# Optimization experiments

Hardware: AMD Instinct MI355X
Metric: run time of the kernel (lower is better)

Reference implementation:

```python
import jax, jax.numpy as jnp
import numpy as np

B, N = 256, 16384


def setup_inputs() -> dict:
    key = jax.random.key(0)
    k1, k2, k3 = jax.random.split(key, 3)
    pred_coords = jax.random.normal(k1, (B, N, 3), dtype=jnp.float32)
    true_coords = jax.random.normal(k2, (B, N, 3), dtype=jnp.float32)
    weights = jax.random.uniform(k3, (B, N), dtype=jnp.float32)
    mask = jnp.ones((B, N), dtype=bool)
    return {"pred_coords": pred_coords, "true_coords": true_coords,
            "weights": weights, "mask": mask}


def reference(pred_coords, true_coords, weights, mask):
    # Mask out invalid atoms (Algorithm 28, weighted Kabsch alignment)
    pred = jnp.where(mask[..., None], pred_coords, 0.0)
    true = jnp.where(mask[..., None], true_coords, 0.0)
    w = jnp.where(mask, weights, 0.0)[..., None]            # [b, n, 1]

    wsum = w.sum(axis=1, keepdims=True)                     # [b, 1, 1]
    pred_centroid = (pred * w).sum(axis=1, keepdims=True) / wsum
    true_centroid = (true * w).sum(axis=1, keepdims=True) / wsum

    pred_c = pred - pred_centroid                           # [b, n, 3]
    true_c = true - true_centroid                           # [b, n, 3]

    # weighted covariance: [b, 3, 3]
    cov = jnp.einsum('bni,bnj->bij', true_c * w, pred_c)

    # torch.svd returns V (not V^T); jnp returns Vh = V^T. rot = U @ V^T = U @ Vh
    U, _, Vh = jnp.linalg.svd(cov)
    rot = jnp.einsum('bij,bjk->bik', U, Vh)

    # reflection fix: flip last column of V (= last row of Vh) where det < 0
    det = jnp.linalg.det(rot)                               # [b]
    flip = jnp.where(det < 0, -1.0, 1.0)                    # [b]
    Vh_fixed = Vh.at[:, -1, :].multiply(flip[:, None])
    rot = jnp.einsum('bij,bjk->bik', U, Vh_fixed)

    aligned = jnp.einsum('bni,bij->bnj', pred_c, rot) + true_centroid
    # original module calls .detach_() on the output
    return jax.lax.stop_gradient(aligned)
```

## Files before the change

### kernel.cpp

```cpp
#include <hip/hip_runtime.h>
#include <stdint.h>
#include <math.h>

constexpr int BATCH  = 256;
constexpr int NATOM  = 16384;
constexpr int CHUNKS = 16;
constexpr int TPB    = 256;
constexpr int APT    = 4;
constexpr int NQ     = 16;

__global__ __launch_bounds__(TPB) void wra_partials(
    const float* __restrict__ pred, const float* __restrict__ tru,
    const float* __restrict__ wgt, const int* __restrict__ mask,
    float* __restrict__ partials)
{
    const int blk = blockIdx.x;
    const int b   = blk >> 4;
    const int s   = blk & 15;
    const int tid = threadIdx.x;
    const long base = (long)b * NATOM + (long)s * (TPB * APT) + (long)tid * APT;

    const float4* p4 = reinterpret_cast<const float4*>(pred + base * 3);
    const float4* t4 = reinterpret_cast<const float4*>(tru  + base * 3);
    float4 pA = p4[0], pB = p4[1], pC = p4[2];
    float4 tA = t4[0], tB = t4[1], tC = t4[2];
    float4 wv = *reinterpret_cast<const float4*>(wgt + base);
    int4   mv = *reinterpret_cast<const int4*>(mask + base);

    float P[12] = {pA.x,pA.y,pA.z,pA.w, pB.x,pB.y,pB.z,pB.w, pC.x,pC.y,pC.z,pC.w};
    float T[12] = {tA.x,tA.y,tA.z,tA.w, tB.x,tB.y,tB.z,tB.w, tC.x,tC.y,tC.z,tC.w};
    float W[4]  = {mv.x ? wv.x : 0.f, mv.y ? wv.y : 0.f,
                   mv.z ? wv.z : 0.f, mv.w ? wv.w : 0.f};

    float acc[NQ];
    #pragma unroll
    for (int k = 0; k < NQ; ++k) acc[k] = 0.f;

    #pragma unroll
    for (int k = 0; k < APT; ++k) {
        float w  = W[k];
        float px = P[3*k], py = P[3*k+1], pz = P[3*k+2];
        float tx = T[3*k], ty = T[3*k+1], tz = T[3*k+2];
        float wtx = w * tx, wty = w * ty, wtz = w * tz;
        acc[0]  += w;
        acc[1]  += w * px;  acc[2]  += w * py;  acc[3]  += w * pz;
        acc[4]  += wtx;     acc[5]  += wty;     acc[6]  += wtz;
        acc[7]  += wtx*px;  acc[8]  += wtx*py;  acc[9]  += wtx*pz;
        acc[10] += wty*px;  acc[11] += wty*py;  acc[12] += wty*pz;
        acc[13] += wtz*px;  acc[14] += wtz*py;  acc[15] += wtz*pz;
    }

    #pragma unroll
    for (int off = 32; off > 0; off >>= 1) {
        #pragma unroll
        for (int k = 0; k < NQ; ++k)
            acc[k] += __shfl_down(acc[k], off, 64);
    }
    __shared__ float red[4][NQ];
    const int wave = tid >> 6, lane = tid & 63;
    if (lane == 0) {
        #pragma unroll
        for (int k = 0; k < NQ; ++k) red[wave][k] = acc[k];
    }
    __syncthreads();
    if (tid < NQ)
        partials[blk * NQ + tid] =
            red[0][tid] + red[1][tid] + red[2][tid] + red[3][tid];
}

__device__ inline void jrot(double M[3][3], double V[3][3], int p, int q) {
    double mpq = M[p][q];
    if (fabs(mpq) < 1e-300) return;
    double theta = (M[q][q] - M[p][p]) / (2.0 * mpq);
    double t = copysign(1.0, theta) / (fabs(theta) + sqrt(theta * theta + 1.0));
    double c = 1.0 / sqrt(t * t + 1.0);
    double s = t * c;
    int r = 3 - p - q;
    double mpp = M[p][p], mqq = M[q][q], mrp = M[r][p], mrq = M[r][q];
    M[p][p] = mpp - t * mpq;
    M[q][q] = mqq + t * mpq;
    M[p][q] = M[q][p] = 0.0;
    double nrp = c * mrp - s * mrq;
    double nrq = s * mrp + c * mrq;
    M[r][p] = M[p][r] = nrp;
    M[r][q] = M[q][r] = nrq;
    #pragma unroll
    for (int i = 0; i < 3; ++i) {
        double vip = V[i][p], viq = V[i][q];
        V[i][p] = c * vip - s * viq;
        V[i][q] = s * vip + c * viq;
    }
}

__global__ __launch_bounds__(64) void wra_solve(
    const float* __restrict__ partials, float* __restrict__ consts)
{
    const int b = blockIdx.x, tid = threadIdx.x;
    __shared__ double q[NQ];
    if (tid < NQ) {
        double sum = 0.0;
        for (int s = 0; s < CHUNKS; ++s)
            sum += (double)partials[(b * CHUNKS + s) * NQ + tid];
        q[tid] = sum;
    }
    __syncthreads();
    if (tid != 0) return;

    double wsum = q[0];
    double pc[3], tc[3];
    for (int j = 0; j < 3; ++j) { pc[j] = q[1+j] / wsum; tc[j] = q[4+j] / wsum; }

    double C[3][3];
    for (int i = 0; i < 3; ++i)
        for (int j = 0; j < 3; ++j)
            C[i][j] = q[7 + 3*i + j] - wsum * tc[i] * pc[j];

    double M[3][3];
    for (int i = 0; i < 3; ++i)
        for (int j = 0; j < 3; ++j)
            M[i][j] = C[0][i]*C[0][j] + C[1][i]*C[1][j] + C[2][i]*C[2][j];
    double V[3][3] = {{1,0,0},{0,1,0},{0,0,1}};
    for (int sweep = 0; sweep < 12; ++sweep) {
        double off = M[0][1]*M[0][1] + M[0][2]*M[0][2] + M[1][2]*M[1][2];
        double diag = M[0][0] + M[1][1] + M[2][2];
        if (off <= 1e-28 * diag * diag) break;
        jrot(M, V, 0, 1);
        jrot(M, V, 0, 2);
        jrot(M, V, 1, 2);
    }
    double lam[3] = {M[0][0], M[1][1], M[2][2]};
    int i0 = 0, i1 = 1, i2 = 2, tmp;
    if (lam[i0] < lam[i1]) { tmp = i0; i0 = i1; i1 = tmp; }
    if (lam[i0] < lam[i2]) { tmp = i0; i0 = i2; i2 = tmp; }
    if (lam[i1] < lam[i2]) { tmp = i1; i1 = i2; i2 = tmp; }
    double v0[3] = {V[0][i0], V[1][i0], V[2][i0]};
    double v1[3] = {V[0][i1], V[1][i1], V[2][i1]};
    double v2[3] = {V[0][i2], V[1][i2], V[2][i2]};

    double u0[3], u1[3];
    for (int i = 0; i < 3; ++i) {
        u0[i] = C[i][0]*v0[0] + C[i][1]*v0[1] + C[i][2]*v0[2];
        u1[i] = C[i][0]*v1[0] + C[i][1]*v1[1] + C[i][2]*v1[2];
    }
    double n0 = sqrt(u0[0]*u0[0] + u0[1]*u0[1] + u0[2]*u0[2]);
    for (int i = 0; i < 3; ++i) u0[i] /= n0;
    double d01 = u1[0]*u0[0] + u1[1]*u0[1] + u1[2]*u0[2];
    for (int i = 0; i < 3; ++i) u1[i] -= d01 * u0[i];
    double n1 = sqrt(u1[0]*u1[0] + u1[1]*u1[1] + u1[2]*u1[2]);
    for (int i = 0; i < 3; ++i) u1[i] /= n1;

    double detV = v0[0]*(v1[1]*v2[2] - v1[2]*v2[1])
                - v0[1]*(v1[0]*v2[2] - v1[2]*v2[0])
                + v0[2]*(v1[0]*v2[1] - v1[1]*v2[0]);
    double sV = (detV >= 0.0) ? 1.0 : -1.0;
    double u2[3] = { sV * (u0[1]*u1[2] - u0[2]*u1[1]),
                     sV * (u0[2]*u1[0] - u0[0]*u1[2]),
                     sV * (u0[0]*u1[1] - u0[1]*u1[0]) };

    float* out = consts + b * 15;
    for (int i = 0; i < 3; ++i)
        for (int j = 0; j < 3; ++j)
            out[3*i + j] = (float)(u0[i]*v0[j] + u1[i]*v1[j] + u2[i]*v2[j]);
    for (int j = 0; j < 3; ++j) { out[9 + j] = (float)pc[j]; out[12 + j] = (float)tc[j]; }
}

__global__ __launch_bounds__(TPB) void wra_apply(
    const float* __restrict__ pred, const int* __restrict__ mask,
    const float* __restrict__ consts, float* __restrict__ out)
{
    const int blk = blockIdx.x;
    const int b   = blk >> 4;
    const int s   = blk & 15;
    const int tid = threadIdx.x;

    __shared__ float c[15];
    if (tid < 15) c[tid] = consts[b * 15 + tid];
    __syncthreads();

    const long base = (long)b * NATOM + (long)s * (TPB * APT) + (long)tid * APT;
    const float4* p4 = reinterpret_cast<const float4*>(pred + base * 3);
    float4 pA = p4[0], pB = p4[1], pC = p4[2];
    int4   mv = *reinterpret_cast<const int4*>(mask + base);

    float P[12] = {pA.x,pA.y,pA.z,pA.w, pB.x,pB.y,pB.z,pB.w, pC.x,pC.y,pC.z,pC.w};
    int Mk[4] = {mv.x, mv.y, mv.z, mv.w};
    float O[12];

    #pragma unroll
    for (int k = 0; k < APT; ++k) {
        float px = (Mk[k] ? P[3*k]   : 0.f) - c[9];
        float py = (Mk[k] ? P[3*k+1] : 0.f) - c[10];
        float pz = (Mk[k] ? P[3*k+2] : 0.f) - c[11];
        O[3*k]   = px * c[0] + py * c[3] + pz * c[6] + c[12];
        O[3*k+1] = px * c[1] + py * c[4] + pz * c[7] + c[13];
        O[3*k+2] = px * c[2] + py * c[5] + pz * c[8] + c[14];
    }
    float4* o4 = reinterpret_cast<float4*>(out + base * 3);
    o4[0] = make_float4(O[0], O[1], O[2],  O[3]);
    o4[1] = make_float4(O[4], O[5], O[6],  O[7]);
    o4[2] = make_float4(O[8], O[9], O[10], O[11]);
}

extern "C" void kernel_launch(void* const* d_in, const int* in_sizes, int n_in,
                              void* d_out, int out_size, void* d_ws, size_t ws_size,
                              hipStream_t stream) {
    const float* pred = (const float*)d_in[0];
    const float* tru  = (const float*)d_in[1];
    const float* wgt  = (const float*)d_in[2];
    const int*   mask = (const int*)d_in[3];
    float* out = (float*)d_out;

    float* partials = (float*)d_ws;
    float* consts   = partials + BATCH * CHUNKS * NQ;

    hipLaunchKernelGGL(wra_partials, dim3(BATCH * CHUNKS), dim3(TPB), 0, stream,
                       pred, tru, wgt, mask, partials);
    hipLaunchKernelGGL(wra_solve, dim3(BATCH), dim3(64), 0, stream,
                       partials, consts);
    hipLaunchKernelGGL(wra_apply, dim3(BATCH * CHUNKS), dim3(TPB), 0, stream,
                       pred, mask, consts, out);
}
```

Baseline: 186.5 us.

## Fuse reduce, solve and apply into one kernel per batch, keeping pred in registers

Replaces the three-kernel pipeline with a single kernel per batch element of 1024 threads. Each thread loads 16 atoms, accumulates the moments and keeps the masked pred coordinates in registers. A thread-0 Jacobi solve runs in shared memory, and then the same threads apply the rotation without re-reading pred or mask. This removes the global partials round trip, two kernel launches and the second read of pred and mask. In exchange only 256 blocks are launched, roughly one per CU, and all other threads of a block sit idle during the serial double-precision solve, so memory-level parallelism and overlap may drop.

Result: slower. 194.7 us (+4.4%).

```diff
diff --git a/kernel.cpp b/kernel.cpp
--- a/kernel.cpp
+++ b/kernel.cpp
@@ -4,69 +4,11 @@
 
 constexpr int BATCH  = 256;
 constexpr int NATOM  = 16384;
-constexpr int CHUNKS = 16;
-constexpr int TPB    = 256;
-constexpr int APT    = 4;
+constexpr int TPB    = 1024;
+constexpr int GROUPS = 4;
 constexpr int NQ     = 16;
-
-__global__ __launch_bounds__(TPB) void wra_partials(
-    const float* __restrict__ pred, const float* __restrict__ tru,
-    const float* __restrict__ wgt, const int* __restrict__ mask,
-    float* __restrict__ partials)
-{
-    const int blk = blockIdx.x;
-    const int b   = blk >> 4;
-    const int s   = blk & 15;
-    const int tid = threadIdx.x;
-    const long base = (long)b * NATOM + (long)s * (TPB * APT) + (long)tid * APT;
-
-    const float4* p4 = reinterpret_cast<const float4*>(pred + base * 3);
-    const float4* t4 = reinterpret_cast<const float4*>(tru  + base * 3);
-    float4 pA = p4[0], pB = p4[1], pC = p4[2];
-    float4 tA = t4[0], tB = t4[1], tC = t4[2];
-    float4 wv = *reinterpret_cast<const float4*>(wgt + base);
-    int4   mv = *reinterpret_cast<const int4*>(mask + base);
-
-    float P[12] = {pA.x,pA.y,pA.z,pA.w, pB.x,pB.y,pB.z,pB.w, pC.x,pC.y,pC.z,pC.w};
-    float T[12] = {tA.x,tA.y,tA.z,tA.w, tB.x,tB.y,tB.z,tB.w, tC.x,tC.y,tC.z,tC.w};
-    float W[4]  = {mv.x ? wv.x : 0.f, mv.y ? wv.y : 0.f,
-                   mv.z ? wv.z : 0.f, mv.w ? wv.w : 0.f};
-
-    float acc[NQ];
-    #pragma unroll
-    for (int k = 0; k < NQ; ++k) acc[k] = 0.f;
-
-    #pragma unroll
-    for (int k = 0; k < APT; ++k) {
-        float w  = W[k];
-        float px = P[3*k], py = P[3*k+1], pz = P[3*k+2];
-        float tx = T[3*k], ty = T[3*k+1], tz = T[3*k+2];
-        float wtx = w * tx, wty = w * ty, wtz = w * tz;
-        acc[0]  += w;
-        acc[1]  += w * px;  acc[2]  += w * py;  acc[3]  += w * pz;
-        acc[4]  += wtx;     acc[5]  += wty;     acc[6]  += wtz;
-        acc[7]  += wtx*px;  acc[8]  += wtx*py;  acc[9]  += wtx*pz;
-        acc[10] += wty*px;  acc[11] += wty*py;  acc[12] += wty*pz;
-        acc[13] += wtz*px;  acc[14] += wtz*py;  acc[15] += wtz*pz;
-    }
-
-    #pragma unroll
-    for (int off = 32; off > 0; off >>= 1) {
-        #pragma unroll
-        for (int k = 0; k < NQ; ++k)
-            acc[k] += __shfl_down(acc[k], off, 64);
-    }
-    __shared__ float red[4][NQ];
-    const int wave = tid >> 6, lane = tid & 63;
-    if (lane == 0) {
-        #pragma unroll
-        for (int k = 0; k < NQ; ++k) red[wave][k] = acc[k];
-    }
-    __syncthreads();
-    if (tid < NQ)
-        partials[blk * NQ + tid] =
-            red[0][tid] + red[1][tid] + red[2][tid] + red[3][tid];
-}
+constexpr int NWAVE  = TPB / 64;
+
 
 __device__ inline void jrot(double M[3][3], double V[3][3], int p, int q) {
     double mpq = M[p][q];
@@ -76,10 +18,10 @@
     double c = 1.0 / sqrt(t * t + 1.0);
     double s = t * c;
     int r = 3 - p - q;
-    double mpp = M[p][p], mqq = M[q][q], mrp = M[r][p], mrq = M[r][q];
-    M[p][p] = mpp - t * mpq;
-    M[q][q] = mqq + t * mpq;
+    M[p][p] -= t * mpq;
+    M[q][q] += t * mpq;
     M[p][q] = M[q][p] = 0.0;
+    double mrp = M[r][p], mrq = M[r][q];
     double nrp = c * mrp - s * mrq;
     double nrq = s * mrp + c * mrq;
     M[r][p] = M[p][r] = nrp;
@@ -92,113 +34,162 @@
     }
 }
 
-__global__ __launch_bounds__(64) void wra_solve(
-    const float* __restrict__ partials, float* __restrict__ consts)
+__global__ __launch_bounds__(TPB) void wra_fused(
+    const float* __restrict__ pred, const float* __restrict__ tru,
+    const float* __restrict__ wgt, const int* __restrict__ mask,
+    float* __restrict__ out)
 {
-    const int b = blockIdx.x, tid = threadIdx.x;
-    __shared__ double q[NQ];
+    const int b   = blockIdx.x;
+    const int tid = threadIdx.x;
+    const long batch0 = (long)b * NATOM;
+
+    float MP[GROUPS][12];
+    float acc[NQ];
+    #pragma unroll
+    for (int k = 0; k < NQ; ++k) acc[k] = 0.f;
+
+    #pragma unroll
+    for (int g = 0; g < GROUPS; ++g) {
+        const long base = batch0 + (long)g * (TPB * 4) + (long)tid * 4;
+        const float4* p4 = reinterpret_cast<const float4*>(pred + base * 3);
+        const float4* t4 = reinterpret_cast<const float4*>(tru  + base * 3);
+        float4 pA = p4[0], pB = p4[1], pC = p4[2];
+        float4 tA = t4[0], tB = t4[1], tC = t4[2];
+        float4 wv = *reinterpret_cast<const float4*>(wgt + base);
+        int4   mv = *reinterpret_cast<const int4*>(mask + base);
+
+        float P[12] = {pA.x,pA.y,pA.z,pA.w, pB.x,pB.y,pB.z,pB.w, pC.x,pC.y,pC.z,pC.w};
+        float T[12] = {tA.x,tA.y,tA.z,tA.w, tB.x,tB.y,tB.z,tB.w, tC.x,tC.y,tC.z,tC.w};
+        int   Mk[4] = {mv.x, mv.y, mv.z, mv.w};
+        float W[4]  = {Mk[0] ? wv.x : 0.f, Mk[1] ? wv.y : 0.f,
+                       Mk[2] ? wv.z : 0.f, Mk[3] ? wv.w : 0.f};
+
+        #pragma unroll
+        for (int k = 0; k < 4; ++k) {
+            float px = Mk[k] ? P[3*k]   : 0.f;
+            float py = Mk[k] ? P[3*k+1] : 0.f;
+            float pz = Mk[k] ? P[3*k+2] : 0.f;
+            MP[g][3*k] = px; MP[g][3*k+1] = py; MP[g][3*k+2] = pz;
+            float w  = W[k];
+            float tx = T[3*k], ty = T[3*k+1], tz = T[3*k+2];
+            float wtx = w * tx, wty = w * ty, wtz = w * tz;
+            acc[0]  += w;
+            acc[1]  += w * px;  acc[2]  += w * py;  acc[3]  += w * pz;
+            acc[4]  += wtx;     acc[5]  += wty;     acc[6]  += wtz;
+            acc[7]  += wtx*px;  acc[8]  += wtx*py;  acc[9]  += wtx*pz;
+            acc[10] += wty*px;  acc[11] += wty*py;  acc[12] += wty*pz;
+            acc[13] += wtz*px;  acc[14] += wtz*py;  acc[15] += wtz*pz;
+        }
+    }
+
+    #pragma unroll
+    for (int off = 32; off > 0; off >>= 1) {
+        #pragma unroll
+        for (int k = 0; k < NQ; ++k)
+            acc[k] += __shfl_down(acc[k], off, 64);
+    }
+    __shared__ float red[NWAVE][NQ];
+    __shared__ double qd[NQ];
+    __shared__ float sc[15];
+    const int wave = tid >> 6, lane = tid & 63;
+    if (lane == 0) {
+        #pragma unroll
+        for (int k = 0; k < NQ; ++k) red[wave][k] = acc[k];
+    }
+    __syncthreads();
     if (tid < NQ) {
         double sum = 0.0;
-        for (int s = 0; s < CHUNKS; ++s)
-            sum += (double)partials[(b * CHUNKS + s) * NQ + tid];
-        q[tid] = sum;
+        #pragma unroll
+        for (int w = 0; w < NWAVE; ++w) sum += (double)red[w][tid];
+        qd[tid] = sum;
     }
     __syncthreads();
-    if (tid != 0) return;
-
-    double wsum = q[0];
-    double pc[3], tc[3];
-    for (int j = 0; j < 3; ++j) { pc[j] = q[1+j] / wsum; tc[j] = q[4+j] / wsum; }
-
-    double C[3][3];
-    for (int i = 0; i < 3; ++i)
-        for (int j = 0; j < 3; ++j)
-            C[i][j] = q[7 + 3*i + j] - wsum * tc[i] * pc[j];
-
-    double M[3][3];
-    for (int i = 0; i < 3; ++i)
-        for (int j = 0; j < 3; ++j)
-            M[i][j] = C[0][i]*C[0][j] + C[1][i]*C[1][j] + C[2][i]*C[2][j];
-    double V[3][3] = {{1,0,0},{0,1,0},{0,0,1}};
-    for (int sweep = 0; sweep < 12; ++sweep) {
-        double off = M[0][1]*M[0][1] + M[0][2]*M[0][2] + M[1][2]*M[1][2];
-        double diag = M[0][0] + M[1][1] + M[2][2];
-        if (off <= 1e-28 * diag * diag) break;
-        jrot(M, V, 0, 1);
-        jrot(M, V, 0, 2);
-        jrot(M, V, 1, 2);
-    }
-    double lam[3] = {M[0][0], M[1][1], M[2][2]};
-    int i0 = 0, i1 = 1, i2 = 2, tmp;
-    if (lam[i0] < lam[i1]) { tmp = i0; i0 = i1; i1 = tmp; }
-    if (lam[i0] < lam[i2]) { tmp = i0; i0 = i2; i2 = tmp; }
-    if (lam[i1] < lam[i2]) { tmp = i1; i1 = i2; i2 = tmp; }
-    double v0[3] = {V[0][i0], V[1][i0], V[2][i0]};
-    double v1[3] = {V[0][i1], V[1][i1], V[2][i1]};
-    double v2[3] = {V[0][i2], V[1][i2], V[2][i2]};
-
-    double u0[3], u1[3];
-    for (int i = 0; i < 3; ++i) {
-        u0[i] = C[i][0]*v0[0] + C[i][1]*v0[1] + C[i][2]*v0[2];
-        u1[i] = C[i][0]*v1[0] + C[i][1]*v1[1] + C[i][2]*v1[2];
-    }
-    double n0 = sqrt(u0[0]*u0[0] + u0[1]*u0[1] + u0[2]*u0[2]);
-    for (int i = 0; i < 3; ++i) u0[i] /= n0;
-    double d01 = u1[0]*u0[0] + u1[1]*u0[1] + u1[2]*u0[2];
-    for (int i = 0; i < 3; ++i) u1[i] -= d01 * u0[i];
-    double n1 = sqrt(u1[0]*u1[0] + u1[1]*u1[1] + u1[2]*u1[2]);
-    for (int i = 0; i < 3; ++i) u1[i] /= n1;
-
-    double detV = v0[0]*(v1[1]*v2[2] - v1[2]*v2[1])
-                - v0[1]*(v1[0]*v2[2] - v1[2]*v2[0])
-                + v0[2]*(v1[0]*v2[1] - v1[1]*v2[0]);
-    double sV = (detV >= 0.0) ? 1.0 : -1.0;
-    double u2[3] = { sV * (u0[1]*u1[2] - u0[2]*u1[1]),
-                     sV * (u0[2]*u1[0] - u0[0]*u1[2]),
-                     sV * (u0[0]*u1[1] - u0[1]*u1[0]) };
-
-    float* out = consts + b * 15;
-    for (int i = 0; i < 3; ++i)
-        for (int j = 0; j < 3; ++j)
-            out[3*i + j] = (float)(u0[i]*v0[j] + u1[i]*v1[j] + u2[i]*v2[j]);
-    for (int j = 0; j < 3; ++j) { out[9 + j] = (float)pc[j]; out[12 + j] = (float)tc[j]; }
-}
-
-__global__ __launch_bounds__(TPB) void wra_apply(
-    const float* __restrict__ pred, const int* __restrict__ mask,
-    const float* __restrict__ consts, float* __restrict__ out)
-{
-    const int blk = blockIdx.x;
-    const int b   = blk >> 4;
-    const int s   = blk & 15;
-    const int tid = threadIdx.x;
-
-    __shared__ float c[15];
-    if (tid < 15) c[tid] = consts[b * 15 + tid];
+
+    if (tid == 0) {
+        double q[NQ];
+        for (int k = 0; k < NQ; ++k) q[k] = qd[k];
+        double wsum = q[0];
+        double pc[3], tc[3];
+        for (int j = 0; j < 3; ++j) { pc[j] = q[1+j] / wsum; tc[j] = q[4+j] / wsum; }
+
+        double C[3][3];
+        for (int i = 0; i < 3; ++i)
+            for (int j = 0; j < 3; ++j)
+                C[i][j] = q[7 + 3*i + j] - wsum * tc[i] * pc[j];
+
+        double M[3][3];
+        for (int i = 0; i < 3; ++i)
+            for (int j = 0; j < 3; ++j)
+                M[i][j] = C[0][i]*C[0][j] + C[1][i]*C[1][j] + C[2][i]*C[2][j];
+        double V[3][3] = {{1,0,0},{0,1,0},{0,0,1}};
+        for (int sweep = 0; sweep < 12; ++sweep) {
+            double off = M[0][1]*M[0][1] + M[0][2]*M[0][2] + M[1][2]*M[1][2];
+            double diag = M[0][0] + M[1][1] + M[2][2];
+            if (off <= 1e-28 * diag * diag) break;
+            jrot(M, V, 0, 1);
+            jrot(M, V, 0, 2);
+            jrot(M, V, 1, 2);
+        }
+        double lam[3] = {M[0][0], M[1][1], M[2][2]};
+        int i0 = 0, i1 = 1, i2 = 2, tmp;
+        if (lam[i0] < lam[i1]) { tmp = i0; i0 = i1; i1 = tmp; }
+        if (lam[i0] < lam[i2]) { tmp = i0; i0 = i2; i2 = tmp; }
+        if (lam[i1] < lam[i2]) { tmp = i1; i1 = i2; i2 = tmp; }
+        double v0[3] = {V[0][i0], V[1][i0], V[2][i0]};
+        double v1[3] = {V[0][i1], V[1][i1], V[2][i1]};
+        double v2[3] = {V[0][i2], V[1][i2], V[2][i2]};
+
+        double u0[3], u1[3];
+        for (int i = 0; i < 3; ++i) {
+            u0[i] = C[i][0]*v0[0] + C[i][1]*v0[1] + C[i][2]*v0[2];
+            u1[i] = C[i][0]*v1[0] + C[i][1]*v1[1] + C[i][2]*v1[2];
+        }
+        double n0 = sqrt(u0[0]*u0[0] + u0[1]*u0[1] + u0[2]*u0[2]);
+        for (int i = 0; i < 3; ++i) u0[i] /= n0;
+        double d01 = u1[0]*u0[0] + u1[1]*u0[1] + u1[2]*u0[2];
+        for (int i = 0; i < 3; ++i) u1[i] -= d01 * u0[i];
+        double n1 = sqrt(u1[0]*u1[0] + u1[1]*u1[1] + u1[2]*u1[2]);
+        for (int i = 0; i < 3; ++i) u1[i] /= n1;
+
+        double detV = v0[0]*(v1[1]*v2[2] - v1[2]*v2[1])
+                    - v0[1]*(v1[0]*v2[2] - v1[2]*v2[0])
+                    + v0[2]*(v1[0]*v2[1] - v1[1]*v2[0]);
+        double sV = (detV >= 0.0) ? 1.0 : -1.0;
+        double u2[3] = { sV * (u0[1]*u1[2] - u0[2]*u1[1]),
+                         sV * (u0[2]*u1[0] - u0[0]*u1[2]),
+                         sV * (u0[0]*u1[1] - u0[1]*u1[0]) };
+
+        for (int i = 0; i < 3; ++i)
+            for (int j = 0; j < 3; ++j)
+                sc[3*i + j] = (float)(u0[i]*v0[j] + u1[i]*v1[j] + u2[i]*v2[j]);
+        for (int j = 0; j < 3; ++j) { sc[9 + j] = (float)pc[j]; sc[12 + j] = (float)tc[j]; }
+    }
     __syncthreads();
 
-    const long base = (long)b * NATOM + (long)s * (TPB * APT) + (long)tid * APT;
-    const float4* p4 = reinterpret_cast<const float4*>(pred + base * 3);
-    float4 pA = p4[0], pB = p4[1], pC = p4[2];
-    int4   mv = *reinterpret_cast<const int4*>(mask + base);
-
-    float P[12] = {pA.x,pA.y,pA.z,pA.w, pB.x,pB.y,pB.z,pB.w, pC.x,pC.y,pC.z,pC.w};
-    int Mk[4] = {mv.x, mv.y, mv.z, mv.w};
-    float O[12];
-
-    #pragma unroll
-    for (int k = 0; k < APT; ++k) {
-        float px = (Mk[k] ? P[3*k]   : 0.f) - c[9];
-        float py = (Mk[k] ? P[3*k+1] : 0.f) - c[10];
-        float pz = (Mk[k] ? P[3*k+2] : 0.f) - c[11];
-        O[3*k]   = px * c[0] + py * c[3] + pz * c[6] + c[12];
-        O[3*k+1] = px * c[1] + py * c[4] + pz * c[7] + c[13];
-        O[3*k+2] = px * c[2] + py * c[5] + pz * c[8] + c[14];
-    }
-    float4* o4 = reinterpret_cast<float4*>(out + base * 3);
-    o4[0] = make_float4(O[0], O[1], O[2],  O[3]);
-    o4[1] = make_float4(O[4], O[5], O[6],  O[7]);
-    o4[2] = make_float4(O[8], O[9], O[10], O[11]);
+    const float c0 = sc[0], c1 = sc[1], c2 = sc[2],
+                c3 = sc[3], c4 = sc[4], c5 = sc[5],
+                c6 = sc[6], c7 = sc[7], c8 = sc[8],
+                pcx = sc[9], pcy = sc[10], pcz = sc[11],
+                tcx = sc[12], tcy = sc[13], tcz = sc[14];
+
+    #pragma unroll
+    for (int g = 0; g < GROUPS; ++g) {
+        const long base = batch0 + (long)g * (TPB * 4) + (long)tid * 4;
+        float O[12];
+        #pragma unroll
+        for (int k = 0; k < 4; ++k) {
+            float px = MP[g][3*k]   - pcx;
+            float py = MP[g][3*k+1] - pcy;
+            float pz = MP[g][3*k+2] - pcz;
+            O[3*k]   = px * c0 + py * c3 + pz * c6 + tcx;
+            O[3*k+1] = px * c1 + py * c4 + pz * c7 + tcy;
+            O[3*k+2] = px * c2 + py * c5 + pz * c8 + tcz;
+        }
+        float4* o4 = reinterpret_cast<float4*>(out + base * 3);
+        o4[0] = make_float4(O[0], O[1], O[2],  O[3]);
+        o4[1] = make_float4(O[4], O[5], O[6],  O[7]);
+        o4[2] = make_float4(O[8], O[9], O[10], O[11]);
+    }
 }
 
 extern "C" void kernel_launch(void* const* d_in, const int* in_sizes, int n_in,
@@ -210,13 +201,6 @@
     const int*   mask = (const int*)d_in[3];
     float* out = (float*)d_out;
 
-    float* partials = (float*)d_ws;
-    float* consts   = partials + BATCH * CHUNKS * NQ;
-
-    hipLaunchKernelGGL(wra_partials, dim3(BATCH * CHUNKS), dim3(TPB), 0, stream,
-                       pred, tru, wgt, mask, partials);
-    hipLaunchKernelGGL(wra_solve, dim3(BATCH), dim3(64), 0, stream,
-                       partials, consts);
-    hipLaunchKernelGGL(wra_apply, dim3(BATCH * CHUNKS), dim3(TPB), 0, stream,
-                       pred, mask, consts, out);
+    hipLaunchKernelGGL(wra_fused, dim3(BATCH), dim3(TPB), 0, stream,
+                       pred, tru, wgt, mask, out);
 }
```
